# Kernel tuning notes

Measured on AMD Instinct MI355X. Metric: run time of the kernel, lower is better.

## Reference

```python
import jax, jax.numpy as jnp
import numpy as np

H, M, D, O, N = 16, 1024, 512, 512, 16384


def setup_inputs() -> dict:
    key = jax.random.key(0)
    ks = jax.random.split(key, 8)
    inp = {
        "k": jax.random.normal(ks[0], (N, O), dtype=jnp.float32),
        "mems": jax.random.normal(ks[1], (H, M, D), dtype=jnp.float32),
        "Wk": jax.random.normal(ks[2], (H, O, D), dtype=jnp.float32) * (1.0 / np.sqrt(D)),
        "bk": jax.random.normal(ks[3], (H, O), dtype=jnp.float32) * 0.02,
        "Wv": jax.random.normal(ks[4], (H, O, D), dtype=jnp.float32) * (1.0 / np.sqrt(D)),
        "bv": jax.random.normal(ks[5], (H, O), dtype=jnp.float32) * 0.02,
        "Wf": jax.random.normal(ks[6], (O, H * O), dtype=jnp.float32) * (1.0 / np.sqrt(H * O)),
        "bf": jax.random.normal(ks[7], (O,), dtype=jnp.float32) * 0.02,
    }
    return inp


def reference(k, mems, Wk, bk, Wv, bv, Wf, bf):
    # Batched over heads. Per head h:
    #   key_h = softmax(mem_h @ Wk_h^T + bk_h)  -> [M, O]
    #   val_h = mem_h @ Wv_h^T + bv_h           -> [M, O]
    #   att_h = softmax(k @ key_h^T)            -> [N, M]
    #   out_h = att_h @ val_h                   -> [N, O]
    key_logits = jnp.einsum("hmd,hod->hmo", mems, Wk) + bk[:, None, :]
    mem_key = jax.nn.softmax(key_logits, axis=-1)            # [H, M, O]
    mem_val = jnp.einsum("hmd,hod->hmo", mems, Wv) + bv[:, None, :]  # [H, M, O]
    att = jnp.einsum("no,hmo->hnm", k, mem_key)              # [H, N, M]
    att_w = jax.nn.softmax(att, axis=-1)
    out_h = jnp.einsum("hnm,hmo->hno", att_w, mem_val)       # [H, N, O]
    # torch.cat(outputs, dim=-1): head h occupies columns [h*O:(h+1)*O]
    x = jnp.transpose(out_h, (1, 0, 2)).reshape(N, H * O)    # [N, H*O]
    return x @ Wf.T + bf                                     # [N, O]
```

## Files before the change

kernel.cpp:

```cpp
#include <hip/hip_runtime.h>
#include <math.h>

typedef unsigned short u16;
typedef __attribute__((ext_vector_type(8))) short short8;
typedef __attribute__((ext_vector_type(4))) float floatx4;

#define Hh 16
#define Mm 1024
#define Dd 512
#define Oo 512
#define Nn 16384

__device__ __forceinline__ float b2f(u16 u) { return __uint_as_float(((unsigned)u) << 16); }
__device__ __forceinline__ u16 f2b(float f) {
    unsigned v = __float_as_uint(f);
    v += 0x7fffu + ((v >> 16) & 1u);
    return (u16)(v >> 16);
}
__device__ __forceinline__ short8 cvt8(const float* p) {
    float4 a = *(const float4*)p, b = *(const float4*)(p + 4);
    u16 o[8];
    o[0] = f2b(a.x); o[1] = f2b(a.y); o[2] = f2b(a.z); o[3] = f2b(a.w);
    o[4] = f2b(b.x); o[5] = f2b(b.y); o[6] = f2b(b.z); o[7] = f2b(b.w);
    return *(short8*)o;
}

__global__ __launch_bounds__(256) void gemm_bt(
    const void* __restrict__ A, const void* __restrict__ B, const float* __restrict__ bias,
    void* __restrict__ C, int K, int lda, int ldb, int ldc,
    long sA, long sB, long sBias, long sC, int aF32, int bF32, int outBf)
{
    __shared__ u16 At[64][72];
    __shared__ u16 Bt[64][72];
    const int tid = threadIdx.x, lane = tid & 63, wid = tid >> 6;
    const int m0 = blockIdx.y * 64, n0 = blockIdx.x * 64;
    const int h = blockIdx.z;
    const int wm = wid >> 1, wn = wid & 1;
    const int rl = lane & 15, rq = (lane >> 4) * 4, gl8 = (lane >> 4) * 8;

    floatx4 zero4 = {0.f, 0.f, 0.f, 0.f};
    floatx4 acc[2][2];
    acc[0][0] = zero4; acc[0][1] = zero4; acc[1][0] = zero4; acc[1][1] = zero4;

    for (int k0 = 0; k0 < K; k0 += 64) {
#pragma unroll
        for (int i = 0; i < 2; i++) {
            int c = tid + i * 256;
            int r = c >> 3, cc = (c & 7) * 8;
            long aoff = (long)h * sA + (long)(m0 + r) * lda + k0 + cc;
            long boff = (long)h * sB + (long)(n0 + r) * ldb + k0 + cc;
            *(short8*)&At[r][cc] = aF32 ? cvt8((const float*)A + aoff)
                                        : *(const short8*)((const u16*)A + aoff);
            *(short8*)&Bt[r][cc] = bF32 ? cvt8((const float*)B + boff)
                                        : *(const short8*)((const u16*)B + boff);
        }
        __syncthreads();
#pragma unroll
        for (int ks = 0; ks < 2; ks++) {
            short8 a0 = *(const short8*)&At[wm * 32 + rl][ks * 32 + gl8];
            short8 a1 = *(const short8*)&At[wm * 32 + 16 + rl][ks * 32 + gl8];
            short8 b0 = *(const short8*)&Bt[wn * 32 + rl][ks * 32 + gl8];
            short8 b1 = *(const short8*)&Bt[wn * 32 + 16 + rl][ks * 32 + gl8];
            acc[0][0] = __builtin_amdgcn_mfma_f32_16x16x32_bf16(a0, b0, acc[0][0], 0, 0, 0);
            acc[0][1] = __builtin_amdgcn_mfma_f32_16x16x32_bf16(a0, b1, acc[0][1], 0, 0, 0);
            acc[1][0] = __builtin_amdgcn_mfma_f32_16x16x32_bf16(a1, b0, acc[1][0], 0, 0, 0);
            acc[1][1] = __builtin_amdgcn_mfma_f32_16x16x32_bf16(a1, b1, acc[1][1], 0, 0, 0);
        }
        __syncthreads();
    }

#pragma unroll
    for (int i = 0; i < 2; i++)
#pragma unroll
        for (int j = 0; j < 2; j++) {
            int col = n0 + wn * 32 + j * 16 + rl;
            float bb = bias ? bias[(long)h * sBias + col] : 0.f;
#pragma unroll
            for (int r = 0; r < 4; r++) {
                int row = m0 + wm * 32 + i * 16 + rq + r;
                long idx = (long)h * sC + (long)row * ldc + col;
                float v = acc[i][j][r] + bb;
                if (outBf) ((u16*)C)[idx] = f2b(v);
                else       ((float*)C)[idx] = v;
            }
        }
}

__global__ __launch_bounds__(256) void softmax_rows(const float* __restrict__ L, u16* __restrict__ Kout)
{
    const int tid = threadIdx.x, lane = tid & 63, wid = tid >> 6;
    const long row = (long)blockIdx.x * 4 + wid;
    const float* p = L + row * 512 + lane * 8;
    float v[8];
    *(float4*)&v[0] = *(const float4*)p;
    *(float4*)&v[4] = *(const float4*)(p + 4);
    float mx = v[0];
#pragma unroll
    for (int i = 1; i < 8; i++) mx = fmaxf(mx, v[i]);
    for (int d = 1; d < 64; d <<= 1) mx = fmaxf(mx, __shfl_xor(mx, d));
    float s = 0.f;
#pragma unroll
    for (int i = 0; i < 8; i++) { v[i] = __expf(v[i] - mx); s += v[i]; }
    for (int d = 1; d < 64; d <<= 1) s += __shfl_xor(s, d);
    float inv = 1.f / s;
    u16 o[8];
#pragma unroll
    for (int i = 0; i < 8; i++) o[i] = f2b(v[i] * inv);
    *(short8*)(Kout + row * 512 + lane * 8) = *(short8*)o;
}

#define LDQ 520
#define LDP 520
#define FLASH_LDS ((64 * LDQ + 64 * LDP) * 2 + 2 * 64 * 4 + 16)

__global__ __launch_bounds__(512, 2) void flash(
    const float* __restrict__ kq, const u16* __restrict__ key,
    const u16* __restrict__ vpt, const float* __restrict__ bfv, float* __restrict__ out)
{
    extern __shared__ u16 sm[];
    u16* kq_s = sm;
    u16* Ph = sm + 64 * LDQ;
    float* lbuf = (float*)(sm + 64 * (LDQ + LDP));

    const int tid = threadIdx.x, lane = tid & 63, wid = tid >> 6;
    const int n0 = blockIdx.x * 64;
    const int rl = lane & 15, rq = (lane >> 4) * 4, gl8 = (lane >> 4) * 8;

#pragma unroll
    for (int i = 0; i < 8; i++) {
        int c = tid + i * 512;
        int r = c >> 6, cc = (c & 63) * 8;
        *(short8*)&kq_s[r * LDQ + cc] = cvt8(&kq[(long)(n0 + r) * 512 + cc]);
    }
    if (tid < 128) lbuf[tid] = 0.f;
    __syncthreads();

    floatx4 zero4 = {0.f, 0.f, 0.f, 0.f};
    floatx4 oacc[4][4], utmp[4][4];
#pragma unroll
    for (int i = 0; i < 4; i++)
#pragma unroll
        for (int j = 0; j < 4; j++) { oacc[i][j] = zero4; utmp[i][j] = zero4; }

    for (int h = 0; h < Hh; h++) {
        const u16* keyh = key + (long)h * Mm * Oo;
        const u16* vph = vpt + (long)h * Oo * Mm;
        float* lcur = lbuf + (h & 1) * 64;
        float* lnxt = lbuf + ((h + 1) & 1) * 64;

        for (int hf = 0; hf < 2; hf++) {
            float psum[4][4];
#pragma unroll
            for (int qt = 0; qt < 4; qt++)
#pragma unroll
                for (int r = 0; r < 4; r++) psum[qt][r] = 0.f;

            for (int t = 0; t < 4; t++) {
                int mb = hf * 512 + wid * 64 + t * 16;
                const u16* bp = keyh + (long)(mb + rl) * 512 + gl8;
                floatx4 s[4];
#pragma unroll
                for (int qt = 0; qt < 4; qt++) s[qt] = zero4;
#pragma unroll
                for (int ks = 0; ks < 16; ks++) {
                    short8 b = *(const short8*)(bp + ks * 32);
#pragma unroll
                    for (int qt = 0; qt < 4; qt++) {
                        short8 a = *(const short8*)&kq_s[(qt * 16 + rl) * LDQ + ks * 32 + gl8];
                        s[qt] = __builtin_amdgcn_mfma_f32_16x16x32_bf16(a, b, s[qt], 0, 0, 0);
                    }
                }
                int colP = wid * 64 + t * 16 + rl;
#pragma unroll
                for (int qt = 0; qt < 4; qt++)
#pragma unroll
                    for (int r = 0; r < 4; r++) {
                        float e = __expf(s[qt][r]);
                        psum[qt][r] += e;
                        Ph[(qt * 16 + rq + r) * LDP + colP] = f2b(e);
                    }
            }
            for (int d = 1; d < 16; d <<= 1)
#pragma unroll
                for (int qt = 0; qt < 4; qt++)
#pragma unroll
                    for (int r = 0; r < 4; r++) psum[qt][r] += __shfl_xor(psum[qt][r], d);
            if (rl == 0)
#pragma unroll
                for (int qt = 0; qt < 4; qt++)
#pragma unroll
                    for (int r = 0; r < 4; r++)
                        atomicAdd(&lcur[qt * 16 + rq + r], psum[qt][r]);
            if (hf == 0 && tid < 64) lnxt[tid] = 0.f;
            __syncthreads();

            const u16* vbp[4];
#pragma unroll
            for (int ot = 0; ot < 4; ot++)
                vbp[ot] = vph + (long)(wid * 64 + ot * 16 + rl) * Mm + hf * 512 + gl8;
#pragma unroll 4
            for (int mk = 0; mk < 16; mk++) {
                short8 a[4], b[4];
#pragma unroll
                for (int qt = 0; qt < 4; qt++)
                    a[qt] = *(const short8*)&Ph[(qt * 16 + rl) * LDP + mk * 32 + gl8];
#pragma unroll
                for (int ot = 0; ot < 4; ot++)
                    b[ot] = *(const short8*)(vbp[ot] + mk * 32);
#pragma unroll
                for (int qt = 0; qt < 4; qt++)
#pragma unroll
                    for (int ot = 0; ot < 4; ot++)
                        utmp[qt][ot] = __builtin_amdgcn_mfma_f32_16x16x32_bf16(a[qt], b[ot], utmp[qt][ot], 0, 0, 0);
            }

            if (hf == 1) {
#pragma unroll
                for (int qt = 0; qt < 4; qt++)
#pragma unroll
                    for (int r = 0; r < 4; r++) {
                        float inv = 1.f / lcur[qt * 16 + rq + r];
#pragma unroll
                        for (int ot = 0; ot < 4; ot++) {
                            oacc[qt][ot][r] += inv * utmp[qt][ot][r];
                            utmp[qt][ot][r] = 0.f;
                        }
                    }
            }
            __syncthreads();
        }
    }

#pragma unroll
    for (int qt = 0; qt < 4; qt++)
#pragma unroll
        for (int ot = 0; ot < 4; ot++) {
            int col = wid * 64 + ot * 16 + rl;
            float add = bfv[col];
#pragma unroll
            for (int r = 0; r < 4; r++) {
                int row = n0 + qt * 16 + rq + r;
                out[(long)row * 512 + col] = oacc[qt][ot][r] + add;
            }
        }
}

extern "C" void kernel_launch(void* const* d_in, const int* in_sizes, int n_in,
                              void* d_out, int out_size, void* d_ws, size_t ws_size,
                              hipStream_t stream)
{
    const float* k    = (const float*)d_in[0];
    const void*  mems = d_in[1];
    const void*  Wk   = d_in[2];
    const float* bk   = (const float*)d_in[3];
    const void*  Wv   = d_in[4];
    const float* bv   = (const float*)d_in[5];
    const void*  Wf   = d_in[6];
    const float* bfv  = (const float*)d_in[7];
    float* out = (float*)d_out;

    char* ws = (char*)d_ws;
    float* logits = (float*)ws;
    u16* keyb = (u16*)(ws + (size_t)Hh * Mm * Oo * 4);
    u16* valb = keyb + (size_t)Hh * Mm * Oo;
    u16* vptb = valb + (size_t)Hh * Mm * Oo;

    gemm_bt<<<dim3(8, 16, 16), 256, 0, stream>>>(
        mems, Wk, bk, logits, 512, 512, 512, 512,
        (long)Mm * Dd, (long)Oo * Dd, 512L, (long)Mm * Oo, 1, 1, 0);

    softmax_rows<<<dim3(Hh * Mm / 4), 256, 0, stream>>>(logits, keyb);

    gemm_bt<<<dim3(8, 16, 16), 256, 0, stream>>>(
        mems, Wv, bv, valb, 512, 512, 512, 512,
        (long)Mm * Dd, (long)Oo * Dd, 512L, (long)Mm * Oo, 1, 1, 1);

    gemm_bt<<<dim3(16, 8, 16), 256, 0, stream>>>(
        Wf, valb, nullptr, vptb, 512, Hh * Oo, 512, 1024,
        512L, (long)Mm * Oo, 0L, (long)Oo * Mm, 1, 0, 1);

    flash<<<dim3(Nn / 64), 512, FLASH_LDS, stream>>>(k, keyb, vptb, bfv, out);
}
```

Before: 1.468 ms.

## Retile flash kernel to 32-row blocks with 16 waves and full-M P buffer

```diff
diff --git a/kernel.cpp b/kernel.cpp
--- a/kernel.cpp
+++ b/kernel.cpp
@@ -110,132 +110,129 @@
 }
 
 #define LDQ 520
-#define LDP 520
-#define FLASH_LDS ((64 * LDQ + 64 * LDP) * 2 + 2 * 64 * 4 + 16)
-
-__global__ __launch_bounds__(512, 2) void flash(
+#define LDP 1032
+#define FLASH_LDS ((32 * LDQ + 32 * LDP) * 2 + 2 * 32 * 4 + 16)
+
+__global__ __launch_bounds__(1024) void flash(
     const float* __restrict__ kq, const u16* __restrict__ key,
     const u16* __restrict__ vpt, const float* __restrict__ bfv, float* __restrict__ out)
 {
     extern __shared__ u16 sm[];
     u16* kq_s = sm;
-    u16* Ph = sm + 64 * LDQ;
-    float* lbuf = (float*)(sm + 64 * (LDQ + LDP));
+    u16* P = sm + 32 * LDQ;
+    float* lbuf = (float*)(sm + 32 * (LDQ + LDP));
 
     const int tid = threadIdx.x, lane = tid & 63, wid = tid >> 6;
-    const int n0 = blockIdx.x * 64;
+    const int n0 = blockIdx.x * 32;
     const int rl = lane & 15, rq = (lane >> 4) * 4, gl8 = (lane >> 4) * 8;
 
 #pragma unroll
-    for (int i = 0; i < 8; i++) {
-        int c = tid + i * 512;
+    for (int i = 0; i < 2; i++) {
+        int c = tid + i * 1024;
         int r = c >> 6, cc = (c & 63) * 8;
         *(short8*)&kq_s[r * LDQ + cc] = cvt8(&kq[(long)(n0 + r) * 512 + cc]);
     }
-    if (tid < 128) lbuf[tid] = 0.f;
+    if (tid < 64) lbuf[tid] = 0.f;
     __syncthreads();
 
     floatx4 zero4 = {0.f, 0.f, 0.f, 0.f};
-    floatx4 oacc[4][4], utmp[4][4];
-#pragma unroll
-    for (int i = 0; i < 4; i++)
-#pragma unroll
-        for (int j = 0; j < 4; j++) { oacc[i][j] = zero4; utmp[i][j] = zero4; }
+    floatx4 oacc[2][2];
+    oacc[0][0] = zero4; oacc[0][1] = zero4; oacc[1][0] = zero4; oacc[1][1] = zero4;
 
     for (int h = 0; h < Hh; h++) {
         const u16* keyh = key + (long)h * Mm * Oo;
         const u16* vph = vpt + (long)h * Oo * Mm;
-        float* lcur = lbuf + (h & 1) * 64;
-        float* lnxt = lbuf + ((h + 1) & 1) * 64;
-
-        for (int hf = 0; hf < 2; hf++) {
-            float psum[4][4];
-#pragma unroll
-            for (int qt = 0; qt < 4; qt++)
+        float* lcur = lbuf + (h & 1) * 32;
+        float* lnxt = lbuf + ((h + 1) & 1) * 32;
+
+        {
+            const int m0 = wid * 64;
+            const u16* bp = keyh + (long)(m0 + rl) * 512 + gl8;
+            floatx4 s[2][4];
+#pragma unroll
+            for (int qt = 0; qt < 2; qt++)
+#pragma unroll
+                for (int t = 0; t < 4; t++) s[qt][t] = zero4;
+
+#pragma unroll 4
+            for (int ks = 0; ks < 16; ks++) {
+                short8 a0 = *(const short8*)&kq_s[rl * LDQ + ks * 32 + gl8];
+                short8 a1 = *(const short8*)&kq_s[(16 + rl) * LDQ + ks * 32 + gl8];
+#pragma unroll
+                for (int t = 0; t < 4; t++) {
+                    short8 b = *(const short8*)(bp + (long)t * 16 * 512 + ks * 32);
+                    s[0][t] = __builtin_amdgcn_mfma_f32_16x16x32_bf16(a0, b, s[0][t], 0, 0, 0);
+                    s[1][t] = __builtin_amdgcn_mfma_f32_16x16x32_bf16(a1, b, s[1][t], 0, 0, 0);
+                }
+            }
+
+            float psum[2][4];
+#pragma unroll
+            for (int qt = 0; qt < 2; qt++)
 #pragma unroll
                 for (int r = 0; r < 4; r++) psum[qt][r] = 0.f;
-
-            for (int t = 0; t < 4; t++) {
-                int mb = hf * 512 + wid * 64 + t * 16;
-                const u16* bp = keyh + (long)(mb + rl) * 512 + gl8;
-                floatx4 s[4];
-#pragma unroll
-                for (int qt = 0; qt < 4; qt++) s[qt] = zero4;
-#pragma unroll
-                for (int ks = 0; ks < 16; ks++) {
-                    short8 b = *(const short8*)(bp + ks * 32);
-#pragma unroll
-                    for (int qt = 0; qt < 4; qt++) {
-                        short8 a = *(const short8*)&kq_s[(qt * 16 + rl) * LDQ + ks * 32 + gl8];
-                        s[qt] = __builtin_amdgcn_mfma_f32_16x16x32_bf16(a, b, s[qt], 0, 0, 0);
+#pragma unroll
+            for (int t = 0; t < 4; t++)
+#pragma unroll
+                for (int qt = 0; qt < 2; qt++)
+#pragma unroll
+                    for (int r = 0; r < 4; r++) {
+                        float e = __expf(s[qt][t][r]);
+                        psum[qt][r] += e;
+                        P[(qt * 16 + rq + r) * LDP + m0 + t * 16 + rl] = f2b(e);
                     }
-                }
-                int colP = wid * 64 + t * 16 + rl;
-#pragma unroll
-                for (int qt = 0; qt < 4; qt++)
-#pragma unroll
-                    for (int r = 0; r < 4; r++) {
-                        float e = __expf(s[qt][r]);
-                        psum[qt][r] += e;
-                        Ph[(qt * 16 + rq + r) * LDP + colP] = f2b(e);
-                    }
-            }
             for (int d = 1; d < 16; d <<= 1)
 #pragma unroll
-                for (int qt = 0; qt < 4; qt++)
+                for (int qt = 0; qt < 2; qt++)
 #pragma unroll
                     for (int r = 0; r < 4; r++) psum[qt][r] += __shfl_xor(psum[qt][r], d);
             if (rl == 0)
 #pragma unroll
-                for (int qt = 0; qt < 4; qt++)
+                for (int qt = 0; qt < 2; qt++)
 #pragma unroll
                     for (int r = 0; r < 4; r++)
                         atomicAdd(&lcur[qt * 16 + rq + r], psum[qt][r]);
-            if (hf == 0 && tid < 64) lnxt[tid] = 0.f;
-            __syncthreads();
-
-            const u16* vbp[4];
-#pragma unroll
-            for (int ot = 0; ot < 4; ot++)
-                vbp[ot] = vph + (long)(wid * 64 + ot * 16 + rl) * Mm + hf * 512 + gl8;
+        }
+        if (tid < 32) lnxt[tid] = 0.f;
+        __syncthreads();
+
+#pragma unroll
+        for (int i = 0; i < 4; i++) {
+            int c = tid + i * 1024;
+            int r = c >> 7, cc = (c & 127) * 8;
+            float inv = 1.f / lcur[r];
+            u16* pp = &P[r * LDP + cc];
+            short8 v = *(short8*)pp;
+            u16 o[8];
+#pragma unroll
+            for (int q = 0; q < 8; q++) o[q] = f2b(b2f(((u16*)&v)[q]) * inv);
+            *(short8*)pp = *(short8*)o;
+        }
+        __syncthreads();
+
+        {
+            const u16* vb0 = vph + (long)(wid * 32 + rl) * Mm + gl8;
+            const u16* vb1 = vph + (long)(wid * 32 + 16 + rl) * Mm + gl8;
 #pragma unroll 4
-            for (int mk = 0; mk < 16; mk++) {
-                short8 a[4], b[4];
-#pragma unroll
-                for (int qt = 0; qt < 4; qt++)
-                    a[qt] = *(const short8*)&Ph[(qt * 16 + rl) * LDP + mk * 32 + gl8];
-#pragma unroll
-                for (int ot = 0; ot < 4; ot++)
-                    b[ot] = *(const short8*)(vbp[ot] + mk * 32);
-#pragma unroll
-                for (int qt = 0; qt < 4; qt++)
-#pragma unroll
-                    for (int ot = 0; ot < 4; ot++)
-                        utmp[qt][ot] = __builtin_amdgcn_mfma_f32_16x16x32_bf16(a[qt], b[ot], utmp[qt][ot], 0, 0, 0);
-            }
-
-            if (hf == 1) {
-#pragma unroll
-                for (int qt = 0; qt < 4; qt++)
-#pragma unroll
-                    for (int r = 0; r < 4; r++) {
-                        float inv = 1.f / lcur[qt * 16 + rq + r];
-#pragma unroll
-                        for (int ot = 0; ot < 4; ot++) {
-                            oacc[qt][ot][r] += inv * utmp[qt][ot][r];
-                            utmp[qt][ot][r] = 0.f;
-                        }
-                    }
-            }
-            __syncthreads();
-        }
+            for (int mk = 0; mk < 32; mk++) {
+                short8 a0 = *(const short8*)&P[rl * LDP + mk * 32 + gl8];
+                short8 a1 = *(const short8*)&P[(16 + rl) * LDP + mk * 32 + gl8];
+                short8 b0 = *(const short8*)(vb0 + mk * 32);
+                short8 b1 = *(const short8*)(vb1 + mk * 32);
+                oacc[0][0] = __builtin_amdgcn_mfma_f32_16x16x32_bf16(a0, b0, oacc[0][0], 0, 0, 0);
+                oacc[0][1] = __builtin_amdgcn_mfma_f32_16x16x32_bf16(a0, b1, oacc[0][1], 0, 0, 0);
+                oacc[1][0] = __builtin_amdgcn_mfma_f32_16x16x32_bf16(a1, b0, oacc[1][0], 0, 0, 0);
+                oacc[1][1] = __builtin_amdgcn_mfma_f32_16x16x32_bf16(a1, b1, oacc[1][1], 0, 0, 0);
+            }
+        }
+        __syncthreads();
     }
 
 #pragma unroll
-    for (int qt = 0; qt < 4; qt++)
-#pragma unroll
-        for (int ot = 0; ot < 4; ot++) {
-            int col = wid * 64 + ot * 16 + rl;
+    for (int qt = 0; qt < 2; qt++)
+#pragma unroll
+        for (int ot = 0; ot < 2; ot++) {
+            int col = wid * 32 + ot * 16 + rl;
             float add = bfv[col];
 #pragma unroll
             for (int r = 0; r < 4; r++) {
@@ -279,5 +276,5 @@
         Wf, valb, nullptr, vptb, 512, Hh * Oo, 512, 1024,
         512L, (long)Mm * Oo, 0L, (long)Oo * Mm, 1, 0, 1);
 
-    flash<<<dim3(Nn / 64), 512, FLASH_LDS, stream>>>(k, keyb, vptb, bfv, out);
-}
+    flash<<<dim3(Nn / 32), 1024, FLASH_LDS, stream>>>(k, keyb, vptb, bfv, out);
+}
```

Result: slower. 2.181 ms (+48.6%).
